# Optimization experiments

Hardware: AMD Instinct MI355X
Metric: run time of the kernel (lower is better)

## Reference

```python
import jax, jax.numpy as jnp
import numpy as np

# db4 (Daubechies-4) lowpass decomposition filter, L = 8 taps
DB4 = np.array([0.23037781330885523, 0.7148465705525415, 0.6308807679295904,
                -0.027983769416983849, -0.18703481171888114, 0.030841381835986965,
                0.032883011666982945, -0.010597401784997278], dtype=np.float32)


def setup_inputs() -> dict:
    key = jax.random.key(0)
    x = jax.random.normal(key, (4, 256, 256, 256), dtype=jnp.float32)
    h = jnp.asarray(DB4)
    return {"x": x, "h": h}


def _corr_valid(u, f):
    # u: [..., T], f: [L]; cross-correlation with VALID padding (== tf.nn.conv1d)
    L = f.shape[0]
    B = int(np.prod(u.shape[:-1]))
    out = jax.lax.conv_general_dilated(
        u.reshape(B, 1, u.shape[-1]), f.reshape(1, 1, L),
        window_strides=(1,), padding='VALID',
        dimension_numbers=('NCW', 'OIW', 'NCW'))
    return out.reshape(u.shape[:-1] + (out.shape[-1],))


def _recon_axis(s, w, h0, h1, axis):
    # s, w: scale / wavelet coefficient halves, same shape; recon along `axis`
    L = h0.shape[0]
    P = (L - 2) // 2 + 1  # number of periodic-wrap samples (= L//2 for even L)
    x = jnp.stack([s, w])                      # [2, ...]
    x = jnp.moveaxis(x, axis + 1, -1)          # bring recon axis to last
    N = x.shape[-1]
    # periodic extension (cyclic gather of last P) then drop first -> len N+P-1
    x = jnp.concatenate([x[..., N - P:], x], axis=-1)[..., 1:]
    # zero-interleaved upsample: [0, x0, 0, x1, ...], then one trailing zero -> len 2N+L-1
    up = jnp.stack([jnp.zeros_like(x), x], axis=-1).reshape(x.shape[:-1] + (-1,))
    up = jnp.pad(up, [(0, 0)] * (up.ndim - 1) + [(0, 1)])
    y = _corr_valid(up[0], h0) + _corr_valid(up[1], h1)  # [..., 2N]
    return jnp.moveaxis(y, -1, axis)


def reference(x, h):
    h0 = h[::-1]                                        # reversed lowpass
    sign = jnp.where(jnp.arange(h.shape[0]) % 2 == 0, -1.0, 1.0).astype(h.dtype)
    h1 = sign * h                                       # QMF highpass (double reverse cancels)
    out = x
    for axis in range(1, x.ndim):
        s, w = jnp.split(out, 2, axis=axis)
        out = _recon_axis(s, w, h0, h1, axis)
    return out
```

## Files before the change

### kernel.cpp

```cpp
#include <hip/hip_runtime.h>


typedef float f32x2 __attribute__((ext_vector_type(2)));

#define FILT_DECL(h)                                          \
  const float a0 = h[6], a1 = h[4], a2 = h[2], a3 = h[0];     \
  const float b0 = h[7], b1 = h[5], b2 = h[3], b3 = h[1];     \
  const float c0 = h[1], c1 = h[3], c2 = h[5], c3 = h[7];     \
  const float d0 = -h[0], d1 = -h[2], d2 = -h[4], d3 = -h[6];

#define Y0(s0,s1,s2,s3,w0,w1,w2,w3)                                        \
  fmaf(w3, c3, fmaf(w2, c2, fmaf(w1, c1, fmaf(w0, c0,                      \
  fmaf(s3, a3, fmaf(s2, a2, fmaf(s1, a1, s0 * a0)))))))
#define Y1(s0,s1,s2,s3,w0,w1,w2,w3)                                        \
  fmaf(w3, d3, fmaf(w2, d2, fmaf(w1, d1, fmaf(w0, d0,                      \
  fmaf(s3, b3, fmaf(s2, b2, fmaf(s1, b1, s0 * b0)))))))

#define PKFMA(s, k, acc) __builtin_elementwise_fma((f32x2){(s),(s)}, (k), (acc))

__global__ __launch_bounds__(256) void wav_axis1_s(const float* __restrict__ in,
                                                   float* __restrict__ tmp,
                                                   const float* __restrict__ h) {
  const int inner = blockIdx.x * 256 + threadIdx.x;
  const int m0 = blockIdx.y * 64;
  const size_t base = (size_t)blockIdx.z * (256u * 65536u) + (unsigned)inner;
  const float* __restrict__ ps = in + base;
  const float* __restrict__ pw = in + base + (size_t)128 * 65536;
  float* __restrict__ po = tmp + base;
  FILT_DECL(h)
  float s0 = __builtin_nontemporal_load(&ps[(size_t)((m0 - 3) & 127) * 65536]);
  float s1 = __builtin_nontemporal_load(&ps[(size_t)((m0 - 2) & 127) * 65536]);
  float s2 = __builtin_nontemporal_load(&ps[(size_t)((m0 - 1) & 127) * 65536]);
  float w0 = __builtin_nontemporal_load(&pw[(size_t)((m0 - 3) & 127) * 65536]);
  float w1 = __builtin_nontemporal_load(&pw[(size_t)((m0 - 2) & 127) * 65536]);
  float w2 = __builtin_nontemporal_load(&pw[(size_t)((m0 - 1) & 127) * 65536]);
  for (int m = m0; m < m0 + 64; ++m) {
    const float s3 = __builtin_nontemporal_load(&ps[(size_t)m * 65536]);
    const float w3 = __builtin_nontemporal_load(&pw[(size_t)m * 65536]);
    po[(size_t)(2 * m) * 65536] = Y0(s0, s1, s2, s3, w0, w1, w2, w3);
    po[(size_t)(2 * m + 1) * 65536] = Y1(s0, s1, s2, s3, w0, w1, w2, w3);
    s0 = s1; s1 = s2; s2 = s3;
    w0 = w1; w1 = w2; w2 = w3;
  }
}

#define RSTR 264
__global__ __launch_bounds__(256) void wav_t23r(const float* __restrict__ tmp,
                                                float* __restrict__ out,
                                                const float* __restrict__ hg) {
  __shared__ __align__(16) float rb[8 * RSTR];
  const int t = threadIdx.x;
  const size_t slice = blockIdx.x >> 1;
  const int m0 = (blockIdx.x & 1) << 6;
  const float* __restrict__ ps = tmp + slice * 65536 + t;
  const float* __restrict__ pw = tmp + slice * 65536 + 32768 + t;
  float* __restrict__ outs = out + slice * 65536;
  FILT_DECL(hg)
  const f32x2 AB0 = {a0, b0}, AB1 = {a1, b1}, AB2 = {a2, b2}, AB3 = {a3, b3};
  const f32x2 CD0 = {c0, d0}, CD1 = {c1, d1}, CD2 = {c2, d2}, CD3 = {c3, d3};
  const int phys = t + ((t < 128) ? 3 : 7);
  const int hcol = (t >= 125 && t < 128) ? (t - 125)
                 : ((t >= 253) ? (t - 121) : -1);
  const int lr = t >> 5;
  const int p0 = (t & 31) << 2;

  float S0 = ps[((m0 - 3) & 127) << 8];
  float S1 = ps[((m0 - 2) & 127) << 8];
  float S2 = ps[((m0 - 1) & 127) << 8];
  float W0 = pw[((m0 - 3) & 127) << 8];
  float W1 = pw[((m0 - 2) & 127) << 8];
  float W2 = pw[((m0 - 1) & 127) << 8];

  for (int ss = 0; ss < 16; ++ss) {
    const int ms = m0 + 4 * ss;
#pragma unroll
    for (int q = 0; q < 4; ++q) {
      const float S3 = ps[(ms + q) << 8];
      const float W3 = pw[(ms + q) << 8];
      f32x2 acc = (f32x2){S0, S0} * AB0;
      acc = PKFMA(S1, AB1, acc);
      acc = PKFMA(S2, AB2, acc);
      acc = PKFMA(S3, AB3, acc);
      acc = PKFMA(W0, CD0, acc);
      acc = PKFMA(W1, CD1, acc);
      acc = PKFMA(W2, CD2, acc);
      acc = PKFMA(W3, CD3, acc);
      rb[(2 * q) * RSTR + phys] = acc.x;
      rb[(2 * q + 1) * RSTR + phys] = acc.y;
      if (hcol >= 0) {
        rb[(2 * q) * RSTR + hcol] = acc.x;
        rb[(2 * q + 1) * RSTR + hcol] = acc.y;
      }
      S0 = S1; S1 = S2; S2 = S3;
      W0 = W1; W1 = W2; W2 = W3;
    }
    __syncthreads();

    const int rbase = lr * RSTR;
    float S[8], W[8];
    {
      const float4 sa = *reinterpret_cast<const float4*>(&rb[rbase + p0]);
      const float4 sb = *reinterpret_cast<const float4*>(&rb[rbase + p0 + 4]);
      S[0]=sa.x; S[1]=sa.y; S[2]=sa.z; S[3]=sa.w;
      S[4]=sb.x; S[5]=sb.y; S[6]=sb.z; S[7]=sb.w;
      const float4 wa = *reinterpret_cast<const float4*>(&rb[rbase + 132 + p0]);
      const float4 wb = *reinterpret_cast<const float4*>(&rb[rbase + 132 + p0 + 4]);
      W[0]=wa.x; W[1]=wa.y; W[2]=wa.z; W[3]=wa.w;
      W[4]=wb.x; W[5]=wb.y; W[6]=wb.z; W[7]=wb.w;
    }
    float* __restrict__ dst = outs + (size_t)(2 * ms + lr) * 256 + 2 * p0;
#pragma unroll
    for (int g = 0; g < 2; ++g) {
      const int k = 2 * g;
      f32x2 eA = (f32x2){S[k], S[k]} * AB0;
      eA = PKFMA(S[k+1], AB1, eA);
      eA = PKFMA(S[k+2], AB2, eA);
      eA = PKFMA(S[k+3], AB3, eA);
      eA = PKFMA(W[k],   CD0, eA);
      eA = PKFMA(W[k+1], CD1, eA);
      eA = PKFMA(W[k+2], CD2, eA);
      eA = PKFMA(W[k+3], CD3, eA);
      f32x2 eB = (f32x2){S[k+1], S[k+1]} * AB0;
      eB = PKFMA(S[k+2], AB1, eB);
      eB = PKFMA(S[k+3], AB2, eB);
      eB = PKFMA(S[k+4], AB3, eB);
      eB = PKFMA(W[k+1], CD0, eB);
      eB = PKFMA(W[k+2], CD1, eB);
      eB = PKFMA(W[k+3], CD2, eB);
      eB = PKFMA(W[k+4], CD3, eB);
      *reinterpret_cast<float4*>(dst + 4 * g) = make_float4(eA.x, eA.y, eB.x, eB.y);
    }
    __syncthreads();
  }
}

__global__ __launch_bounds__(256) void wav_axis1(const float* __restrict__ in,
                                                 float* __restrict__ out,
                                                 const float* __restrict__ h) {
  const int inner = blockIdx.x * 256 + threadIdx.x;
  const int m0 = blockIdx.y * 64;
  const size_t base = (size_t)blockIdx.z * (256u * 65536u) + (unsigned)inner;
  const float* __restrict__ ps = in + base;
  const float* __restrict__ pw = in + base + (size_t)128 * 65536;
  float* __restrict__ po = out + base;
  FILT_DECL(h)
  float s0 = ps[(size_t)((m0 - 3) & 127) * 65536];
  float s1 = ps[(size_t)((m0 - 2) & 127) * 65536];
  float s2 = ps[(size_t)((m0 - 1) & 127) * 65536];
  float w0 = pw[(size_t)((m0 - 3) & 127) * 65536];
  float w1 = pw[(size_t)((m0 - 2) & 127) * 65536];
  float w2 = pw[(size_t)((m0 - 1) & 127) * 65536];
  for (int m = m0; m < m0 + 64; ++m) {
    const float s3 = ps[(size_t)m * 65536];
    const float w3 = pw[(size_t)m * 65536];
    po[(size_t)(2 * m) * 65536] = Y0(s0, s1, s2, s3, w0, w1, w2, w3);
    po[(size_t)(2 * m + 1) * 65536] = Y1(s0, s1, s2, s3, w0, w1, w2, w3);
    s0 = s1; s1 = s2; s2 = s3;
    w0 = w1; w1 = w2; w2 = w3;
  }
}

__global__ __launch_bounds__(256) void wav_axis2(float* __restrict__ buf,
                                                 const float* __restrict__ h) {
  __shared__ float tile[256][32];
  const int t = threadIdx.x;
  const int c = t & 31;
  const int g = t >> 5;
  const size_t slice = (size_t)(blockIdx.x >> 3);
  const int col0 = (blockIdx.x & 7) * 32;
  float* __restrict__ p = buf + slice * 65536 + col0;
#pragma unroll
  for (int i = 0; i < 32; ++i) {
    const int rr = i * 8 + g;
    tile[rr][c] = p[rr * 256 + c];
  }
  __syncthreads();
  FILT_DECL(h)
  const int m0 = g * 16;
  float s0 = tile[(m0 - 3) & 127][c];
  float s1 = tile[(m0 - 2) & 127][c];
  float s2 = tile[(m0 - 1) & 127][c];
  float w0 = tile[128 + ((m0 - 3) & 127)][c];
  float w1 = tile[128 + ((m0 - 2) & 127)][c];
  float w2 = tile[128 + ((m0 - 1) & 127)][c];
#pragma unroll
  for (int m = m0; m < m0 + 16; ++m) {
    const float s3 = tile[m][c];
    const float w3 = tile[128 + m][c];
    p[(2 * m) * 256 + c] = Y0(s0, s1, s2, s3, w0, w1, w2, w3);
    p[(2 * m + 1) * 256 + c] = Y1(s0, s1, s2, s3, w0, w1, w2, w3);
    s0 = s1; s1 = s2; s2 = s3;
    w0 = w1; w1 = w2; w2 = w3;
  }
}

__global__ __launch_bounds__(256) void wav_axis3(float* __restrict__ buf,
                                                 const float* __restrict__ h) {
  __shared__ float tile[512];
  const int t = threadIdx.x;
  float* __restrict__ p = buf + (size_t)blockIdx.x * 512;
  tile[t] = p[t];
  tile[256 + t] = p[256 + t];
  __syncthreads();
  FILT_DECL(h)
  const int rr = t >> 7;
  const int m = t & 127;
  const float* __restrict__ line = tile + rr * 256;
  const float s0 = line[(m - 3) & 127];
  const float s1 = line[(m - 2) & 127];
  const float s2 = line[(m - 1) & 127];
  const float s3 = line[m];
  const float w0 = line[128 + ((m - 3) & 127)];
  const float w1 = line[128 + ((m - 2) & 127)];
  const float w2 = line[128 + ((m - 1) & 127)];
  const float w3 = line[128 + m];
  float2 y;
  y.x = Y0(s0, s1, s2, s3, w0, w1, w2, w3);
  y.y = Y1(s0, s1, s2, s3, w0, w1, w2, w3);
  *reinterpret_cast<float2*>(p + rr * 256 + 2 * m) = y;
}

extern "C" void kernel_launch(void* const* d_in, const int* in_sizes, int n_in,
                              void* d_out, int out_size, void* d_ws, size_t ws_size,
                              hipStream_t stream) {
  const float* x = (const float*)d_in[0];
  const float* h = (const float*)d_in[1];
  float* out = (float*)d_out;
  const size_t need = (size_t)4 * 256 * 256 * 256 * 4;

  if (ws_size >= need) {
    float* tmp = (float*)d_ws;
    wav_axis1_s<<<dim3(256, 2, 4), 256, 0, stream>>>(x, tmp, h);
    wav_t23r<<<dim3(2048), 256, 0, stream>>>(tmp, out, h);
  } else {
    wav_axis1<<<dim3(256, 2, 4), 256, 0, stream>>>(x, out, h);
    wav_axis2<<<dim3(8192), 256, 0, stream>>>(out, h);
    wav_axis3<<<dim3(131072), 256, 0, stream>>>(out, h);
  }
}
```

Baseline: 232.7 us.

## Regroup axis passes: fuse axes 1 and 3, run axis 2 separately

Instead of axis 1 alone followed by a fused axis-2/axis-3 kernel, the first kernel now reconstructs along axis 1 and axis 3 together, using LDS for the contiguous last axis. A second kernel then does axis 2 with a streaming per-slice pass. Both passes still read and write the full tensor once through the workspace, so the aim is a better access pattern and balance between the two kernels. The risk is that the first kernel's strided loads 64K floats apart may coalesce worse than before.

```diff
diff --git a/kernel.cpp b/kernel.cpp
--- a/kernel.cpp
+++ b/kernel.cpp
@@ -18,43 +18,18 @@
 
 #define PKFMA(s, k, acc) __builtin_elementwise_fma((f32x2){(s),(s)}, (k), (acc))
 
-__global__ __launch_bounds__(256) void wav_axis1_s(const float* __restrict__ in,
-                                                   float* __restrict__ tmp,
-                                                   const float* __restrict__ h) {
-  const int inner = blockIdx.x * 256 + threadIdx.x;
+#define RSTR 264
+__global__ __launch_bounds__(256) void wav_a13(const float* __restrict__ in,
+                                               float* __restrict__ tmp,
+                                               const float* __restrict__ hg) {
+  __shared__ __align__(16) float rb[8 * RSTR];
+  const int t = threadIdx.x;
+  const int col2 = blockIdx.x;
   const int m0 = blockIdx.y * 64;
-  const size_t base = (size_t)blockIdx.z * (256u * 65536u) + (unsigned)inner;
-  const float* __restrict__ ps = in + base;
-  const float* __restrict__ pw = in + base + (size_t)128 * 65536;
-  float* __restrict__ po = tmp + base;
-  FILT_DECL(h)
-  float s0 = __builtin_nontemporal_load(&ps[(size_t)((m0 - 3) & 127) * 65536]);
-  float s1 = __builtin_nontemporal_load(&ps[(size_t)((m0 - 2) & 127) * 65536]);
-  float s2 = __builtin_nontemporal_load(&ps[(size_t)((m0 - 1) & 127) * 65536]);
-  float w0 = __builtin_nontemporal_load(&pw[(size_t)((m0 - 3) & 127) * 65536]);
-  float w1 = __builtin_nontemporal_load(&pw[(size_t)((m0 - 2) & 127) * 65536]);
-  float w2 = __builtin_nontemporal_load(&pw[(size_t)((m0 - 1) & 127) * 65536]);
-  for (int m = m0; m < m0 + 64; ++m) {
-    const float s3 = __builtin_nontemporal_load(&ps[(size_t)m * 65536]);
-    const float w3 = __builtin_nontemporal_load(&pw[(size_t)m * 65536]);
-    po[(size_t)(2 * m) * 65536] = Y0(s0, s1, s2, s3, w0, w1, w2, w3);
-    po[(size_t)(2 * m + 1) * 65536] = Y1(s0, s1, s2, s3, w0, w1, w2, w3);
-    s0 = s1; s1 = s2; s2 = s3;
-    w0 = w1; w1 = w2; w2 = w3;
-  }
-}
-
-#define RSTR 264
-__global__ __launch_bounds__(256) void wav_t23r(const float* __restrict__ tmp,
-                                                float* __restrict__ out,
-                                                const float* __restrict__ hg) {
-  __shared__ __align__(16) float rb[8 * RSTR];
-  const int t = threadIdx.x;
-  const size_t slice = blockIdx.x >> 1;
-  const int m0 = (blockIdx.x & 1) << 6;
-  const float* __restrict__ ps = tmp + slice * 65536 + t;
-  const float* __restrict__ pw = tmp + slice * 65536 + 32768 + t;
-  float* __restrict__ outs = out + slice * 65536;
+  const size_t bb = (size_t)blockIdx.z * 16777216;
+  const float* __restrict__ ps = in + bb + col2 * 256 + t;
+  const float* __restrict__ pw = ps + (size_t)128 * 65536;
+  float* __restrict__ tout = tmp + bb + col2 * 256;
   FILT_DECL(hg)
   const f32x2 AB0 = {a0, b0}, AB1 = {a1, b1}, AB2 = {a2, b2}, AB3 = {a3, b3};
   const f32x2 CD0 = {c0, d0}, CD1 = {c1, d1}, CD2 = {c2, d2}, CD3 = {c3, d3};
@@ -64,19 +39,19 @@
   const int lr = t >> 5;
   const int p0 = (t & 31) << 2;
 
-  float S0 = ps[((m0 - 3) & 127) << 8];
-  float S1 = ps[((m0 - 2) & 127) << 8];
-  float S2 = ps[((m0 - 1) & 127) << 8];
-  float W0 = pw[((m0 - 3) & 127) << 8];
-  float W1 = pw[((m0 - 2) & 127) << 8];
-  float W2 = pw[((m0 - 1) & 127) << 8];
+  float S0 = __builtin_nontemporal_load(&ps[(size_t)((m0 - 3) & 127) * 65536]);
+  float S1 = __builtin_nontemporal_load(&ps[(size_t)((m0 - 2) & 127) * 65536]);
+  float S2 = __builtin_nontemporal_load(&ps[(size_t)((m0 - 1) & 127) * 65536]);
+  float W0 = __builtin_nontemporal_load(&pw[(size_t)((m0 - 3) & 127) * 65536]);
+  float W1 = __builtin_nontemporal_load(&pw[(size_t)((m0 - 2) & 127) * 65536]);
+  float W2 = __builtin_nontemporal_load(&pw[(size_t)((m0 - 1) & 127) * 65536]);
 
   for (int ss = 0; ss < 16; ++ss) {
     const int ms = m0 + 4 * ss;
 #pragma unroll
     for (int q = 0; q < 4; ++q) {
-      const float S3 = ps[(ms + q) << 8];
-      const float W3 = pw[(ms + q) << 8];
+      const float S3 = __builtin_nontemporal_load(&ps[(size_t)(ms + q) * 65536]);
+      const float W3 = __builtin_nontemporal_load(&pw[(size_t)(ms + q) * 65536]);
       f32x2 acc = (f32x2){S0, S0} * AB0;
       acc = PKFMA(S1, AB1, acc);
       acc = PKFMA(S2, AB2, acc);
@@ -108,7 +83,7 @@
       W[0]=wa.x; W[1]=wa.y; W[2]=wa.z; W[3]=wa.w;
       W[4]=wb.x; W[5]=wb.y; W[6]=wb.z; W[7]=wb.w;
     }
-    float* __restrict__ dst = outs + (size_t)(2 * ms + lr) * 256 + 2 * p0;
+    float* __restrict__ dst = tout + (size_t)(2 * ms + lr) * 65536 + 2 * p0;
 #pragma unroll
     for (int g = 0; g < 2; ++g) {
       const int k = 2 * g;
@@ -134,6 +109,32 @@
   }
 }
 
+__global__ __launch_bounds__(256) void wav_b2(const float* __restrict__ tmp,
+                                              float* __restrict__ out,
+                                              const float* __restrict__ h) {
+  const int t = threadIdx.x;
+  const int m0 = blockIdx.y * 64;
+  const size_t slice = blockIdx.x;
+  const float* __restrict__ ps = tmp + slice * 65536 + t;
+  const float* __restrict__ pw = ps + 32768;
+  float* __restrict__ po = out + slice * 65536 + t;
+  FILT_DECL(h)
+  float s0 = __builtin_nontemporal_load(&ps[((m0 - 3) & 127) * 256]);
+  float s1 = __builtin_nontemporal_load(&ps[((m0 - 2) & 127) * 256]);
+  float s2 = __builtin_nontemporal_load(&ps[((m0 - 1) & 127) * 256]);
+  float w0 = __builtin_nontemporal_load(&pw[((m0 - 3) & 127) * 256]);
+  float w1 = __builtin_nontemporal_load(&pw[((m0 - 2) & 127) * 256]);
+  float w2 = __builtin_nontemporal_load(&pw[((m0 - 1) & 127) * 256]);
+  for (int m = m0; m < m0 + 64; ++m) {
+    const float s3 = __builtin_nontemporal_load(&ps[m * 256]);
+    const float w3 = __builtin_nontemporal_load(&pw[m * 256]);
+    po[(2 * m) * 256] = Y0(s0, s1, s2, s3, w0, w1, w2, w3);
+    po[(2 * m + 1) * 256] = Y1(s0, s1, s2, s3, w0, w1, w2, w3);
+    s0 = s1; s1 = s2; s2 = s3;
+    w0 = w1; w1 = w2; w2 = w3;
+  }
+}
+
 __global__ __launch_bounds__(256) void wav_axis1(const float* __restrict__ in,
                                                  float* __restrict__ out,
                                                  const float* __restrict__ h) {
@@ -230,8 +231,8 @@
 
   if (ws_size >= need) {
     float* tmp = (float*)d_ws;
-    wav_axis1_s<<<dim3(256, 2, 4), 256, 0, stream>>>(x, tmp, h);
-    wav_t23r<<<dim3(2048), 256, 0, stream>>>(tmp, out, h);
+    wav_a13<<<dim3(256, 2, 4), 256, 0, stream>>>(x, tmp, h);
+    wav_b2<<<dim3(1024, 2), 256, 0, stream>>>(tmp, out, h);
   } else {
     wav_axis1<<<dim3(256, 2, 4), 256, 0, stream>>>(x, out, h);
     wav_axis2<<<dim3(8192), 256, 0, stream>>>(out, h);
```

Measured after the change: 226.6 us. 1.03x faster.
